# Performance work log

Measured on AMD Instinct MI355X. Metric: run time of the kernel, lower is better.

The kernel has to match this reference:

```python
import jax, jax.numpy as jnp
import numpy as np

T, B, D_IN, D_H, D_OUT = 16, 8192, 512, 1024, 256


def setup_inputs() -> dict:
    key = jax.random.key(0)
    ks = jax.random.split(key, 4)
    # He-style scaled init to keep activations sane
    x = jax.random.normal(ks[0], (B, D_IN), dtype=jnp.float32)
    W1 = jax.random.normal(ks[1], (T, D_IN, D_H), dtype=jnp.float32) / np.sqrt(D_IN)
    b1 = jnp.zeros((T, D_H), dtype=jnp.float32)
    W2 = jax.random.normal(ks[2], (T, D_H, D_H), dtype=jnp.float32) / np.sqrt(D_H)
    b2 = jnp.zeros((T, D_H), dtype=jnp.float32)
    W3 = jax.random.normal(ks[3], (T, D_H, D_OUT), dtype=jnp.float32) / np.sqrt(D_H)
    b3 = jnp.zeros((T, D_OUT), dtype=jnp.float32)
    return {"x": x, "W1": W1, "b1": b1, "W2": W2, "b2": b2, "W3": W3, "b3": b3}


def reference(x, W1, b1, W2, b2, W3, b3):
    # Batched over the tree dimension t: one grouped GEMM per layer instead of
    # a Python loop over trees.
    h = jax.nn.relu(jnp.einsum('bi,tih->tbh', x, W1) + b1[:, None, :])   # [T,B,H]
    h = jax.nn.relu(jnp.einsum('tbh,thk->tbk', h, W2) + b2[:, None, :])  # [T,B,H]
    out = jnp.einsum('tbh,tho->tbo', h, W3) + b3[:, None, :]             # [T,B,O]
    return jnp.mean(out, axis=0)                                          # [B,O]
```

## Files before the change

### kernel.cpp

```cpp
#include <hip/hip_runtime.h>
#include <hip/hip_bf16.h>
#include <stdint.h>

#define T_TREES 16
#define B_ROWS  8192
#define DIN     512
#define DH      1024
#define DOUT    256

typedef unsigned short u16;
typedef __attribute__((ext_vector_type(8))) short short8;
typedef __attribute__((ext_vector_type(16))) float floatx16;

__device__ __forceinline__ u16 f2bf(float f) {
    union { float f; uint32_t u; } v; v.f = f;
    uint32_t u = v.u;
    uint32_t r = (u + 0x7fffu + ((u >> 16) & 1u)) >> 16;
    return (u16)r;
}

__device__ __forceinline__ void async_copy16(const u16* g, u16* l) {
    __builtin_amdgcn_global_load_lds(
        (const __attribute__((address_space(1))) uint32_t*)g,
        (__attribute__((address_space(3))) uint32_t*)l,
        16, 0, 0);
}

__global__ void prep_kernel(const float* __restrict__ x, u16* __restrict__ xb,
                            const float* __restrict__ b3, float* __restrict__ out,
                            const float* __restrict__ W1, const float* __restrict__ W2,
                            const float* __restrict__ W3,
                            u16* __restrict__ W1b, u16* __restrict__ W2b,
                            u16* __restrict__ W3b) {
    __shared__ float tile[32][33];
    if (blockIdx.x < 4096) {
        int idx = blockIdx.x * 256 + threadIdx.x;
        float4 v = ((const float4*)x)[idx];
        ushort4 o;
        o.x = f2bf(v.x); o.y = f2bf(v.y); o.z = f2bf(v.z); o.w = f2bf(v.w);
        ((ushort4*)xb)[idx] = o;
    } else if (blockIdx.x < 12288) {
        int idx = (blockIdx.x - 4096) * 256 + threadIdx.x;
        int o = idx & (DOUT - 1);
        float s = 0.f;
#pragma unroll
        for (int t = 0; t < T_TREES; t++) s += b3[t * DOUT + o];
        out[idx] = s * (1.f / T_TREES);
    } else {
        int bid = blockIdx.x - 12288;
        int t = bid / 1792, tl = bid - t * 1792;
        const float* in; u16* outp; int K, N, kt, nt; float scale = 1.f;
        if (tl < 512)       { in = W1; outp = W1b; K = DIN; N = DH;   kt = tl & 15; nt = tl >> 4; }
        else if (tl < 1536) { tl -= 512;  in = W2; outp = W2b; K = DH; N = DH;   kt = tl & 31; nt = tl >> 5; }
        else                { tl -= 1536; in = W3; outp = W3b; K = DH; N = DOUT; kt = tl & 31; nt = tl >> 5;
                              scale = 1.f / T_TREES; }
        int k0 = kt * 32, n0 = nt * 32;
        const float* inb = in + (size_t)t * K * N;
        u16* outb = outp + (size_t)t * K * N;
        int c = threadIdx.x & 31, rg = threadIdx.x >> 5;
#pragma unroll
        for (int i = 0; i < 4; i++) {
            int r = rg * 4 + i;
            tile[r][c] = inb[(size_t)(k0 + r) * N + n0 + c];
        }
        __syncthreads();
#pragma unroll
        for (int i = 0; i < 4; i++) {
            int r = rg * 4 + i;
            outb[(size_t)(n0 + r) * K + k0 + c] = f2bf(tile[c][r] * scale);
        }
    }
}

__global__ void reduce_kernel(const float* __restrict__ Part, float* __restrict__ Out, int g) {
    int idx = blockIdx.x * 256 + threadIdx.x;
    float4 s = ((const float4*)Out)[idx];
    for (int t = 0; t < g; t++) {
        float4 p = ((const float4*)(Part + (size_t)t * B_ROWS * DOUT))[idx];
        s.x += p.x; s.y += p.y; s.z += p.z; s.w += p.w;
    }
    ((float4*)Out)[idx] = s;
}


#define GEMM_PREAMBLE()                                          \
    const int tid = threadIdx.x;                                 \
    const int wave = tid >> 6;                                   \
    const int lane = tid & 63;                                   \
    const int l31 = lane & 31;                                   \
    const int h = lane >> 5;                                     \
    const int rb = l31 & 3;                                      \
    const int wm = (wave >> 1) * 64;                             \
    const int wn = (wave & 1) * 64;                              \
    const int s = lane >> 3;                                     \
    const int c8 = lane & 7;                                     \
    const int colElem = ((c8 ^ ((s & 3) << 1)) << 3);

#define GEMM_KSLAB(Ab, Bb, K)                                                         \
    {                                                                                  \
        _Pragma("unroll")                                                              \
        for (int i = 0; i < 4; i++) {                                                  \
            const int j = wave * 4 + i;                                                \
            const int r = j * 8 + s;                                                   \
            async_copy16(Ab + (size_t)(m0 + r) * K + kk + colElem, &ldsA[j * 512]);    \
            async_copy16(Bb + (size_t)(n0 + r) * K + kk + colElem, &ldsB[j * 512]);    \
        }                                                                              \
        __syncthreads();                                                               \
        _Pragma("unroll")                                                              \
        for (int kq = 0; kq < 4; kq++) {                                               \
            const int col = ((kq ^ rb) << 4) + h * 8;                                  \
            short8 a[2], b[2];                                                         \
            _Pragma("unroll")                                                          \
            for (int fi = 0; fi < 2; fi++)                                             \
                a[fi] = *(const short8*)&ldsA[(wm + fi * 32 + l31) * 64 + col];        \
            _Pragma("unroll")                                                          \
            for (int fj = 0; fj < 2; fj++)                                             \
                b[fj] = *(const short8*)&ldsB[(wn + fj * 32 + l31) * 64 + col];        \
            _Pragma("unroll")                                                          \
            for (int fi = 0; fi < 2; fi++)                                             \
                _Pragma("unroll")                                                      \
                for (int fj = 0; fj < 2; fj++)                                         \
                    acc[fi][fj] = __builtin_amdgcn_mfma_f32_32x32x16_bf16(             \
                        a[fi], b[fj], acc[fi][fj], 0, 0, 0);                           \
        }                                                                              \
        __syncthreads();                                                               \
    }

__global__ __launch_bounds__(256, 2)
void gemm_relu_bf16(const u16* __restrict__ A, size_t aStrideT,
                    const u16* __restrict__ Bt,
                    const float* __restrict__ bias,
                    u16* __restrict__ C,
                    int M, int N, int K) {
    __shared__ u16 ldsA[128 * 64];
    __shared__ u16 ldsB[128 * 64];

    const int t = blockIdx.z;
    const u16* Ab = A + (size_t)t * aStrideT;
    const u16* Bb = Bt + (size_t)t * (size_t)N * K;
    u16* Cb = C + (size_t)t * (size_t)M * N;
    const float* biasb = bias + (size_t)t * N;

    const int m0 = blockIdx.x * 128;
    const int n0 = blockIdx.y * 128;

    GEMM_PREAMBLE();

    floatx16 acc[2][2];
#pragma unroll
    for (int fi = 0; fi < 2; fi++)
#pragma unroll
        for (int fj = 0; fj < 2; fj++)
#pragma unroll
            for (int r = 0; r < 16; r++) acc[fi][fj][r] = 0.f;

    for (int kk = 0; kk < K; kk += 64) GEMM_KSLAB(Ab, Bb, K);

#pragma unroll
    for (int fj = 0; fj < 2; fj++) {
        const int n = n0 + wn + fj * 32 + l31;
        const float bv = biasb[n];
#pragma unroll
        for (int fi = 0; fi < 2; fi++) {
#pragma unroll
            for (int r = 0; r < 16; r++) {
                const int m = m0 + wm + fi * 32 + (r & 3) + 8 * (r >> 2) + 4 * h;
                float v = acc[fi][fj][r] + bv;
                v = v > 0.f ? v : 0.f;
                Cb[(size_t)m * N + n] = f2bf(v);
            }
        }
    }
}

__global__ __launch_bounds__(256, 2)
void gemm_final_part(const u16* __restrict__ H2, const u16* __restrict__ W3t,
                     float* __restrict__ Part) {
    constexpr int M = B_ROWS, N = DOUT, K = DH;
    __shared__ u16 ldsA[128 * 64];
    __shared__ u16 ldsB[128 * 64];

    const int m0 = blockIdx.x * 128;
    const int n0 = blockIdx.y * 128;
    const int t = blockIdx.z;
    const u16* Ab = H2 + (size_t)t * M * K;
    const u16* Bb = W3t + (size_t)t * N * K;
    float* Pb = Part + (size_t)t * M * N;

    GEMM_PREAMBLE();

    floatx16 acc[2][2];
#pragma unroll
    for (int fi = 0; fi < 2; fi++)
#pragma unroll
        for (int fj = 0; fj < 2; fj++)
#pragma unroll
            for (int r = 0; r < 16; r++) acc[fi][fj][r] = 0.f;

    for (int kk = 0; kk < K; kk += 64) GEMM_KSLAB(Ab, Bb, K);

#pragma unroll
    for (int fj = 0; fj < 2; fj++) {
        const int n = n0 + wn + fj * 32 + l31;
#pragma unroll
        for (int fi = 0; fi < 2; fi++) {
#pragma unroll
            for (int r = 0; r < 16; r++) {
                const int m = m0 + wm + fi * 32 + (r & 3) + 8 * (r >> 2) + 4 * h;
                Pb[(size_t)m * N + n] = acc[fi][fj][r];
            }
        }
    }
}

extern "C" void kernel_launch(void* const* d_in, const int* in_sizes, int n_in,
                              void* d_out, int out_size, void* d_ws, size_t ws_size,
                              hipStream_t stream) {
    const float* x  = (const float*)d_in[0];
    const float* W1 = (const float*)d_in[1];
    const float* b1 = (const float*)d_in[2];
    const float* W2 = (const float*)d_in[3];
    const float* b2 = (const float*)d_in[4];
    const float* W3 = (const float*)d_in[5];
    const float* b3 = (const float*)d_in[6];
    float* out = (float*)d_out;

    const size_t XB_BYTES = 8388608ull;
    const size_t W1B_BYTES = 16777216ull, W2B_BYTES = 33554432ull, W3B_BYTES = 8388608ull;
    const size_t FIXED = XB_BYTES + W1B_BYTES + W2B_BYTES + W3B_BYTES;
    const size_t PER_TREE = 33554432ull;

    uint8_t* ws = (uint8_t*)d_ws;
    u16* xb  = (u16*)ws;
    u16* W1b = (u16*)(ws + XB_BYTES);
    u16* W2b = (u16*)(ws + XB_BYTES + W1B_BYTES);
    u16* W3b = (u16*)(ws + XB_BYTES + W1B_BYTES + W2B_BYTES);
    u16* h1  = (u16*)(ws + FIXED);
    float* part = (float*)(ws + FIXED);

    int g = 16;
    while (g > 1 && FIXED + (size_t)g * PER_TREE > ws_size) g >>= 1;
    const int nG = T_TREES / g;
    u16* h2 = (u16*)(ws + FIXED + (size_t)g * (PER_TREE / 2));

    prep_kernel<<<12288 + 1792 * T_TREES, 256, 0, stream>>>(
        x, xb, b3, out, W1, W2, W3, W1b, W2b, W3b);

    for (int gi = 0; gi < nG; gi++) {
        const int t0 = gi * g;
        gemm_relu_bf16<<<dim3(B_ROWS / 128, DH / 128, g), 256, 0, stream>>>(
            xb, 0, W1b + (size_t)t0 * DIN * DH, b1 + (size_t)t0 * DH, h1, B_ROWS, DH, DIN);
        gemm_relu_bf16<<<dim3(B_ROWS / 128, DH / 128, g), 256, 0, stream>>>(
            h1, (size_t)B_ROWS * DH, W2b + (size_t)t0 * DH * DH, b2 + (size_t)t0 * DH, h2, B_ROWS, DH, DH);
        gemm_final_part<<<dim3(B_ROWS / 128, DOUT / 128, g), 256, 0, stream>>>(
            h2, W3b + (size_t)t0 * DH * DOUT, part);
        reduce_kernel<<<(B_ROWS * DOUT / 4) / 256, 256, 0, stream>>>(part, out, g);
    }
}
```

Baseline: 820.6 us.

## Fuse layer-2 and layer-3 GEMMs, keeping h2 in LDS and accumulating across trees

Replaces the separate layer-2 GEMM and final GEMM with one kernel. Each block computes a 128x128 h2 tile with bias and ReLU into LDS, multiplies it by the matching W3 slice, and loops over trees while keeping the output accumulators in registers. This removes the h2 round trip through global memory and the per-tree partial writes. Eight partial planes, one per layer-2 column block, are summed by a fixed 8-way reduce. It also raises the occupancy hint on the layer-1 GEMM. The costs are a higher LDS footprint and register pressure, far fewer blocks each running a longer serial loop over trees, and un-overlapped W3 loads.

Measured after the change: 1.020 ms. 24.3% more time.

```diff
diff --git a/kernel.cpp b/kernel.cpp
--- a/kernel.cpp
+++ b/kernel.cpp
@@ -72,12 +72,13 @@
     }
 }
 
-__global__ void reduce_kernel(const float* __restrict__ Part, float* __restrict__ Out, int g) {
+__global__ void reduce_kernel(const float* __restrict__ Planes, float* __restrict__ Out) {
     int idx = blockIdx.x * 256 + threadIdx.x;
     float4 s = ((const float4*)Out)[idx];
-    for (int t = 0; t < g; t++) {
-        float4 p = ((const float4*)(Part + (size_t)t * B_ROWS * DOUT))[idx];
-        s.x += p.x; s.y += p.y; s.z += p.z; s.w += p.w;
+#pragma unroll
+    for (int p = 0; p < 8; p++) {
+        float4 v = ((const float4*)(Planes + (size_t)p * B_ROWS * DOUT))[idx];
+        s.x += v.x; s.y += v.y; s.z += v.z; s.w += v.w;
     }
     ((float4*)Out)[idx] = s;
 }
@@ -126,7 +127,7 @@
         __syncthreads();                                                               \
     }
 
-__global__ __launch_bounds__(256, 2)
+__global__ __launch_bounds__(256, 4)
 void gemm_relu_bf16(const u16* __restrict__ A, size_t aStrideT,
                     const u16* __restrict__ Bt,
                     const float* __restrict__ bias,
@@ -174,40 +175,111 @@
 }
 
 __global__ __launch_bounds__(256, 2)
-void gemm_final_part(const u16* __restrict__ H2, const u16* __restrict__ W3t,
-                     float* __restrict__ Part) {
-    constexpr int M = B_ROWS, N = DOUT, K = DH;
+void gemm_l2_final(const u16* __restrict__ H1, const u16* __restrict__ W2b,
+                   const float* __restrict__ b2, const u16* __restrict__ W3b,
+                   float* __restrict__ Planes, int t0, int g) {
+    constexpr int M = B_ROWS, K = DH, N3 = DOUT, K3 = DH;
     __shared__ u16 ldsA[128 * 64];
     __shared__ u16 ldsB[128 * 64];
+    __shared__ u16 h2t[128 * 128];
+    __shared__ u16 w3buf[128 * 64];
 
     const int m0 = blockIdx.x * 128;
     const int n0 = blockIdx.y * 128;
-    const int t = blockIdx.z;
-    const u16* Ab = H2 + (size_t)t * M * K;
-    const u16* Bb = W3t + (size_t)t * N * K;
-    float* Pb = Part + (size_t)t * M * N;
 
     GEMM_PREAMBLE();
 
-    floatx16 acc[2][2];
-#pragma unroll
-    for (int fi = 0; fi < 2; fi++)
-#pragma unroll
-        for (int fj = 0; fj < 2; fj++)
-#pragma unroll
-            for (int r = 0; r < 16; r++) acc[fi][fj][r] = 0.f;
-
-    for (int kk = 0; kk < K; kk += 64) GEMM_KSLAB(Ab, Bb, K);
-
-#pragma unroll
-    for (int fj = 0; fj < 2; fj++) {
-        const int n = n0 + wn + fj * 32 + l31;
-#pragma unroll
-        for (int fi = 0; fi < 2; fi++) {
-#pragma unroll
-            for (int r = 0; r < 16; r++) {
-                const int m = m0 + wm + fi * 32 + (r & 3) + 8 * (r >> 2) + 4 * h;
-                Pb[(size_t)m * N + n] = acc[fi][fj][r];
+    floatx16 acc2[2][2][2];
+#pragma unroll
+    for (int p = 0; p < 2; p++)
+#pragma unroll
+        for (int fi = 0; fi < 2; fi++)
+#pragma unroll
+            for (int fj = 0; fj < 2; fj++)
+#pragma unroll
+                for (int r = 0; r < 16; r++) acc2[p][fi][fj][r] = 0.f;
+
+    for (int tt = 0; tt < g; tt++) {
+        const int t = t0 + tt;
+        const u16* Ab = H1 + (size_t)tt * M * K;
+        const u16* Bb = W2b + (size_t)t * K * K;
+        const float* biasb = b2 + (size_t)t * DH;
+        const u16* W3t = W3b + (size_t)t * N3 * K3;
+
+        floatx16 acc[2][2];
+#pragma unroll
+        for (int fi = 0; fi < 2; fi++)
+#pragma unroll
+            for (int fj = 0; fj < 2; fj++)
+#pragma unroll
+                for (int r = 0; r < 16; r++) acc[fi][fj][r] = 0.f;
+
+        for (int kk = 0; kk < K; kk += 64) GEMM_KSLAB(Ab, Bb, K);
+
+#pragma unroll
+        for (int fj = 0; fj < 2; fj++) {
+            const int kcol = wn + fj * 32 + l31;
+            const float bv = biasb[n0 + kcol];
+#pragma unroll
+            for (int fi = 0; fi < 2; fi++) {
+#pragma unroll
+                for (int r = 0; r < 16; r++) {
+                    const int m = wm + fi * 32 + (r & 3) + 8 * (r >> 2) + 4 * h;
+                    float v = acc[fi][fj][r] + bv;
+                    v = v > 0.f ? v : 0.f;
+                    h2t[m * 128 + (kcol ^ ((m & 3) << 4))] = f2bf(v);
+                }
+            }
+        }
+        __syncthreads();
+
+#pragma unroll
+        for (int pass = 0; pass < 2; pass++) {
+#pragma unroll
+            for (int slab = 0; slab < 2; slab++) {
+#pragma unroll
+                for (int i = 0; i < 4; i++) {
+                    const int j = wave * 4 + i;
+                    const int rr = pass * 128 + j * 8 + s;
+                    async_copy16(W3t + (size_t)rr * K3 + n0 + slab * 64 + colElem,
+                                 &w3buf[j * 512]);
+                }
+                __syncthreads();
+#pragma unroll
+                for (int kq = 0; kq < 4; kq++) {
+                    const int col = ((kq ^ rb) << 4) + h * 8;
+                    short8 a[2], b[2];
+#pragma unroll
+                    for (int fi = 0; fi < 2; fi++)
+                        a[fi] = *(const short8*)&h2t[(wm + fi * 32 + l31) * 128 + slab * 64 + col];
+#pragma unroll
+                    for (int fj = 0; fj < 2; fj++)
+                        b[fj] = *(const short8*)&w3buf[(wn + fj * 32 + l31) * 64 + col];
+#pragma unroll
+                    for (int fi = 0; fi < 2; fi++)
+#pragma unroll
+                        for (int fj = 0; fj < 2; fj++)
+                            acc2[pass][fi][fj] = __builtin_amdgcn_mfma_f32_32x32x16_bf16(
+                                a[fi], b[fj], acc2[pass][fi][fj], 0, 0, 0);
+                }
+                __syncthreads();
+            }
+        }
+    }
+
+    float* Pb = Planes + (size_t)blockIdx.y * M * N3;
+#pragma unroll
+    for (int pass = 0; pass < 2; pass++) {
+#pragma unroll
+        for (int fj = 0; fj < 2; fj++) {
+            const int n = pass * 128 + wn + fj * 32 + l31;
+#pragma unroll
+            for (int fi = 0; fi < 2; fi++) {
+#pragma unroll
+                for (int r = 0; r < 16; r++) {
+                    const int m = m0 + wm + fi * 32 + (r & 3) + 8 * (r >> 2) + 4 * h;
+                    Pb[(size_t)m * N3 + n] = acc2[pass][fi][fj][r];
+                }
             }
         }
     }
@@ -228,7 +300,8 @@
     const size_t XB_BYTES = 8388608ull;
     const size_t W1B_BYTES = 16777216ull, W2B_BYTES = 33554432ull, W3B_BYTES = 8388608ull;
     const size_t FIXED = XB_BYTES + W1B_BYTES + W2B_BYTES + W3B_BYTES;
-    const size_t PER_TREE = 33554432ull;
+    const size_t PER_TREE = 16777216ull;
+    const size_t PLANES_BYTES = 67108864ull;
 
     uint8_t* ws = (uint8_t*)d_ws;
     u16* xb  = (u16*)ws;
@@ -236,12 +309,11 @@
     u16* W2b = (u16*)(ws + XB_BYTES + W1B_BYTES);
     u16* W3b = (u16*)(ws + XB_BYTES + W1B_BYTES + W2B_BYTES);
     u16* h1  = (u16*)(ws + FIXED);
-    float* part = (float*)(ws + FIXED);
 
     int g = 16;
-    while (g > 1 && FIXED + (size_t)g * PER_TREE > ws_size) g >>= 1;
+    while (g > 1 && FIXED + (size_t)g * PER_TREE + PLANES_BYTES > ws_size) g >>= 1;
     const int nG = T_TREES / g;
-    u16* h2 = (u16*)(ws + FIXED + (size_t)g * (PER_TREE / 2));
+    float* planes = (float*)(ws + FIXED + (size_t)g * PER_TREE);
 
     prep_kernel<<<12288 + 1792 * T_TREES, 256, 0, stream>>>(
         x, xb, b3, out, W1, W2, W3, W1b, W2b, W3b);
@@ -250,10 +322,8 @@
         const int t0 = gi * g;
         gemm_relu_bf16<<<dim3(B_ROWS / 128, DH / 128, g), 256, 0, stream>>>(
             xb, 0, W1b + (size_t)t0 * DIN * DH, b1 + (size_t)t0 * DH, h1, B_ROWS, DH, DIN);
-        gemm_relu_bf16<<<dim3(B_ROWS / 128, DH / 128, g), 256, 0, stream>>>(
-            h1, (size_t)B_ROWS * DH, W2b + (size_t)t0 * DH * DH, b2 + (size_t)t0 * DH, h2, B_ROWS, DH, DH);
-        gemm_final_part<<<dim3(B_ROWS / 128, DOUT / 128, g), 256, 0, stream>>>(
-            h2, W3b + (size_t)t0 * DH * DOUT, part);
-        reduce_kernel<<<(B_ROWS * DOUT / 4) / 256, 256, 0, stream>>>(part, out, g);
-    }
-}
+        gemm_l2_final<<<dim3(B_ROWS / 128, DH / 128), 256, 0, stream>>>(
+            h1, W2b, b2, W3b, planes, t0, g);
+        reduce_kernel<<<(B_ROWS * DOUT / 4) / 256, 256, 0, stream>>>(planes, out);
+    }
+}
```

## Register-prefetch next K slab to overlap global loads with MFMA compute

Applied to the files above, without the earlier changes.

Replaces the direct global-to-LDS async copies with loads into registers. The next K slab is prefetched while the current slab is computed, then written to LDS behind a barrier. This is meant to hide global memory latency that was previously exposed between the load and the compute of each slab. In exchange it adds register pressure from 8 short8 prefetch registers and an extra LDS write pass, and it gives up the direct-to-LDS load path.

New measurement: 890.2 us. +8.5%, slower.

```diff
diff --git a/kernel.cpp b/kernel.cpp
--- a/kernel.cpp
+++ b/kernel.cpp
@@ -17,13 +17,6 @@
     uint32_t u = v.u;
     uint32_t r = (u + 0x7fffu + ((u >> 16) & 1u)) >> 16;
     return (u16)r;
-}
-
-__device__ __forceinline__ void async_copy16(const u16* g, u16* l) {
-    __builtin_amdgcn_global_load_lds(
-        (const __attribute__((address_space(1))) uint32_t*)g,
-        (__attribute__((address_space(3))) uint32_t*)l,
-        16, 0, 0);
 }
 
 __global__ void prep_kernel(const float* __restrict__ x, u16* __restrict__ xb,
@@ -72,12 +65,12 @@
     }
 }
 
-__global__ void reduce_kernel(const float* __restrict__ Part, float* __restrict__ Out, int g) {
+__global__ void reduce_kernel(const float* __restrict__ Part, float* __restrict__ Out, int np) {
     int idx = blockIdx.x * 256 + threadIdx.x;
     float4 s = ((const float4*)Out)[idx];
-    for (int t = 0; t < g; t++) {
-        float4 p = ((const float4*)(Part + (size_t)t * B_ROWS * DOUT))[idx];
-        s.x += p.x; s.y += p.y; s.z += p.z; s.w += p.w;
+    for (int p = 0; p < np; p++) {
+        float4 v = ((const float4*)(Part + (size_t)p * B_ROWS * DOUT))[idx];
+        s.x += v.x; s.y += v.y; s.z += v.z; s.w += v.w;
     }
     ((float4*)Out)[idx] = s;
 }
@@ -96,34 +89,58 @@
     const int c8 = lane & 7;                                     \
     const int colElem = ((c8 ^ ((s & 3) << 1)) << 3);
 
-#define GEMM_KSLAB(Ab, Bb, K)                                                         \
-    {                                                                                  \
-        _Pragma("unroll")                                                              \
-        for (int i = 0; i < 4; i++) {                                                  \
-            const int j = wave * 4 + i;                                                \
-            const int r = j * 8 + s;                                                   \
-            async_copy16(Ab + (size_t)(m0 + r) * K + kk + colElem, &ldsA[j * 512]);    \
-            async_copy16(Bb + (size_t)(n0 + r) * K + kk + colElem, &ldsB[j * 512]);    \
-        }                                                                              \
-        __syncthreads();                                                               \
-        _Pragma("unroll")                                                              \
-        for (int kq = 0; kq < 4; kq++) {                                               \
-            const int col = ((kq ^ rb) << 4) + h * 8;                                  \
-            short8 a[2], b[2];                                                         \
-            _Pragma("unroll")                                                          \
-            for (int fi = 0; fi < 2; fi++)                                             \
-                a[fi] = *(const short8*)&ldsA[(wm + fi * 32 + l31) * 64 + col];        \
-            _Pragma("unroll")                                                          \
-            for (int fj = 0; fj < 2; fj++)                                             \
-                b[fj] = *(const short8*)&ldsB[(wn + fj * 32 + l31) * 64 + col];        \
-            _Pragma("unroll")                                                          \
-            for (int fi = 0; fi < 2; fi++)                                             \
-                _Pragma("unroll")                                                      \
-                for (int fj = 0; fj < 2; fj++)                                         \
-                    acc[fi][fj] = __builtin_amdgcn_mfma_f32_32x32x16_bf16(             \
-                        a[fi], b[fj], acc[fi][fj], 0, 0, 0);                           \
-        }                                                                              \
-        __syncthreads();                                                               \
+#define GEMM_LOAD(Ab, Bb, K, kk)                                                        \
+    {                                                                                    \
+        _Pragma("unroll")                                                                \
+        for (int i = 0; i < 4; i++) {                                                    \
+            const int j = wave * 4 + i;                                                  \
+            pa[i] = *(const short8*)(Ab + (size_t)(m0 + j * 8 + s) * K + (kk) + colElem);\
+            pb[i] = *(const short8*)(Bb + (size_t)(n0 + j * 8 + s) * K + (kk) + colElem);\
+        }                                                                                \
+    }
+
+#define GEMM_WRITE()                                                                    \
+    {                                                                                    \
+        _Pragma("unroll")                                                                \
+        for (int i = 0; i < 4; i++) {                                                    \
+            const int j = wave * 4 + i;                                                  \
+            *(short8*)&ldsA[j * 512 + lane * 8] = pa[i];                                 \
+            *(short8*)&ldsB[j * 512 + lane * 8] = pb[i];                                 \
+        }                                                                                \
+    }
+
+#define GEMM_COMPUTE()                                                                  \
+    {                                                                                    \
+        _Pragma("unroll")                                                                \
+        for (int kq = 0; kq < 4; kq++) {                                                 \
+            const int col = ((kq ^ rb) << 4) + h * 8;                                    \
+            short8 a[2], b[2];                                                           \
+            _Pragma("unroll")                                                            \
+            for (int fi = 0; fi < 2; fi++)                                               \
+                a[fi] = *(const short8*)&ldsA[(wm + fi * 32 + l31) * 64 + col];          \
+            _Pragma("unroll")                                                            \
+            for (int fj = 0; fj < 2; fj++)                                               \
+                b[fj] = *(const short8*)&ldsB[(wn + fj * 32 + l31) * 64 + col];          \
+            _Pragma("unroll")                                                            \
+            for (int fi = 0; fi < 2; fi++)                                               \
+                _Pragma("unroll")                                                        \
+                for (int fj = 0; fj < 2; fj++)                                           \
+                    acc[fi][fj] = __builtin_amdgcn_mfma_f32_32x32x16_bf16(               \
+                        a[fi], b[fj], acc[fi][fj], 0, 0, 0);                             \
+        }                                                                                \
+    }
+
+#define GEMM_KLOOP(Ab, Bb, K, kStart, kEnd)                                             \
+    {                                                                                    \
+        short8 pa[4], pb[4];                                                             \
+        GEMM_LOAD(Ab, Bb, K, kStart);                                                    \
+        for (int kk = kStart; kk < kEnd; kk += 64) {                                     \
+            if (kk > kStart) __syncthreads();                                            \
+            GEMM_WRITE();                                                                \
+            __syncthreads();                                                             \
+            if (kk + 64 < kEnd) GEMM_LOAD(Ab, Bb, K, kk + 64);                           \
+            GEMM_COMPUTE();                                                              \
+        }                                                                                \
     }
 
 __global__ __launch_bounds__(256, 2)
@@ -154,7 +171,7 @@
 #pragma unroll
             for (int r = 0; r < 16; r++) acc[fi][fj][r] = 0.f;
 
-    for (int kk = 0; kk < K; kk += 64) GEMM_KSLAB(Ab, Bb, K);
+    GEMM_KLOOP(Ab, Bb, K, 0, K);
 
 #pragma unroll
     for (int fj = 0; fj < 2; fj++) {
@@ -197,7 +214,7 @@
 #pragma unroll
             for (int r = 0; r < 16; r++) acc[fi][fj][r] = 0.f;
 
-    for (int kk = 0; kk < K; kk += 64) GEMM_KSLAB(Ab, Bb, K);
+    GEMM_KLOOP(Ab, Bb, K, 0, K);
 
 #pragma unroll
     for (int fj = 0; fj < 2; fj++) {
```
